# Optimization experiments

Measured on AMD Instinct MI355X. Metric: run time of the kernel, lower is better.

Reference implementation:

```python
import jax, jax.numpy as jnp
import numpy as np

B, NQ, NK = 2, 2048, 2048
QD, CD, H, DH = 1024, 768, 16, 64
INNER = H * DH


def setup_inputs() -> dict:
    key = jax.random.key(0)
    ks = jax.random.split(key, 8)
    x = jax.random.normal(ks[0], (B, NQ, QD), jnp.float32)
    context = jax.random.normal(ks[1], (B, NK, CD), jnp.float32)
    mask = jax.random.randint(ks[2], (B, 1, NQ, NK), 0, 2) > 0
    s = lambda d: 1.0 / np.sqrt(d)
    Wq = jax.random.normal(ks[3], (INNER, QD), jnp.float32) * s(QD)
    Wk = jax.random.normal(ks[4], (INNER, CD), jnp.float32) * s(CD)
    Wv = jax.random.normal(ks[5], (INNER, CD), jnp.float32) * s(CD)
    Wo = jax.random.normal(ks[6], (QD, INNER), jnp.float32) * s(INNER)
    bo = jax.random.normal(ks[7], (QD,), jnp.float32) * 0.01
    return {"x": x, "context": context, "mask": mask,
            "Wq": Wq, "Wk": Wk, "Wv": Wv, "Wo": Wo, "bo": bo}


def reference(x, context, mask, Wq, Wk, Wv, Wo, bo):
    scale = DH ** -0.5
    # QKV projections (Linear, no bias): [b, n, inner] -> [b, n, h, d]
    q = (x @ Wq.T).reshape(B, NQ, H, DH)
    k = (context @ Wk.T).reshape(B, NK, H, DH)
    v = (context @ Wv.T).reshape(B, NK, H, DH)
    # additive bias built from boolean mask (masked_fill with -finfo.max/2)
    max_neg = -jnp.finfo(q.dtype).max / 2
    bias = jnp.where(mask, jnp.zeros((), q.dtype), max_neg)  # [b,1,nq,nk]
    scores = jnp.einsum('bqhd,bkhd->bhqk', q, k) * scale + bias
    attn = jax.nn.softmax(scores, axis=-1)
    out = jnp.einsum('bhqk,bkhd->bqhd', attn, v).reshape(B, NQ, INNER)
    return out @ Wo.T + bo
```

## Files before the change

### kernel.cpp

```cpp
#include <hip/hip_runtime.h>
#include <float.h>
#include <stdint.h>

#define C_B     2
#define C_NQ    2048
#define C_NK    2048
#define C_QD    1024
#define C_CD    768
#define C_H     16
#define C_DH    64
#define C_INNER 1024

typedef __bf16 bf16;
typedef __attribute__((ext_vector_type(8))) __bf16 bf16x8;
typedef __attribute__((ext_vector_type(4))) __bf16 bf16x4;
typedef __attribute__((ext_vector_type(4))) float f32x4;
typedef __attribute__((ext_vector_type(16))) float f32x16;

#if __has_builtin(__builtin_amdgcn_exp2f)
#define EXP2(x) __builtin_amdgcn_exp2f(x)
#else
#define EXP2(x) __expf((x) * 0.69314718056f)
#endif

__device__ __forceinline__ void async_copy16(const bf16* g, bf16* l) {
  __builtin_amdgcn_global_load_lds(
      (const __attribute__((address_space(1))) void*)g,
      (__attribute__((address_space(3))) void*)l,
      16, 0, 0);
}

__global__ __launch_bounds__(256) void cvt_all(const float* __restrict__ s0, const float* __restrict__ s1,
                                               const float* __restrict__ s2, const float* __restrict__ s3,
                                               const float* __restrict__ s4, const float* __restrict__ s5,
                                               bf16* __restrict__ d0, bf16* __restrict__ d1,
                                               bf16* __restrict__ d2, bf16* __restrict__ d3,
                                               bf16* __restrict__ d4, bf16* __restrict__ d5) {
  const int stride = gridDim.x * blockDim.x;
  for (int idx = blockIdx.x * blockDim.x + threadIdx.x; idx < 2752512; idx += stride) {
    const float* src; bf16* dst; int loc;
    if      (idx < 1048576) { src = s0; dst = d0; loc = idx; }
    else if (idx < 1835008) { src = s1; dst = d1; loc = idx - 1048576; }
    else if (idx < 2097152) { src = s2; dst = d2; loc = idx - 1835008; }
    else if (idx < 2293760) { src = s3; dst = d3; loc = idx - 2097152; }
    else if (idx < 2490368) { src = s4; dst = d4; loc = idx - 2293760; }
    else                    { src = s5; dst = d5; loc = idx - 2490368; }
    float4 f = *(const float4*)&src[loc * 4];
    bf16x4 o = { (bf16)f.x, (bf16)f.y, (bf16)f.z, (bf16)f.w };
    *(bf16x4*)&dst[loc * 4] = o;
  }
}

__global__ __launch_bounds__(256) void pack_mask(const int* __restrict__ mask,
                                                 unsigned long long* __restrict__ mb,
                                                 int nwords) {
  const int wid  = (blockIdx.x * blockDim.x + threadIdx.x) >> 6;
  const int lane = threadIdx.x & 63;
  const int nw   = (gridDim.x * blockDim.x) >> 6;
  for (int w = wid; w < nwords; w += nw) {
    int v = mask[(size_t)w * 64 + lane];
    unsigned long long bb = __ballot(v != 0);
    if (lane == 0) mb[w] = bb;
  }
}

template <int OUTBF16, int HASBIAS>
__global__ __launch_bounds__(256) void gemm_bt(const bf16* __restrict__ A,
                                               const bf16* __restrict__ W,
                                               const float* __restrict__ bias,
                                               void* __restrict__ Cout,
                                               int M, int N, int K, float oscale,
                                               int ncut, bf16* __restrict__ Cout2) {
  __shared__ __align__(16) bf16 As[2][64 * 32];
  __shared__ __align__(16) bf16 Bs[2][128 * 32];

  const int t = threadIdx.x;
  const int w = t >> 6, lane = t & 63;
  const int l15 = lane & 15, lg = lane >> 4;
  const int wm = w >> 1, wn = w & 1;
  const int m0 = blockIdx.y * 64, n0 = blockIdx.x * 128;

  f32x4 acc[2][4] = {};

  const bf16* Ag  = A + (size_t)(m0 + w * 16 + (lane >> 2)) * K + (lane & 3) * 8;
  const bf16* Bg0 = W + (size_t)(n0 + w * 32 + (lane >> 2)) * K + (lane & 3) * 8;
  const bf16* Bg1 = W + (size_t)(n0 + w * 32 + 16 + (lane >> 2)) * K + (lane & 3) * 8;

  auto stage = [&](int nb, int k0) {
    async_copy16(Ag + k0, &As[nb][w * 512]);
    async_copy16(Bg0 + k0, &Bs[nb][w * 1024]);
    async_copy16(Bg1 + k0, &Bs[nb][w * 1024 + 512]);
  };

  stage(0, 0);
  int cur = 0;
  for (int k0 = 0; k0 < K; k0 += 32) {
    __syncthreads();
    if (k0 + 32 < K) stage(cur ^ 1, k0 + 32);

    bf16x8 af[2], bfv[4];
#pragma unroll
    for (int mi = 0; mi < 2; ++mi)
      af[mi] = *(const bf16x8*)&As[cur][(wm * 32 + mi * 16 + l15) * 32 + lg * 8];
#pragma unroll
    for (int ni = 0; ni < 4; ++ni)
      bfv[ni] = *(const bf16x8*)&Bs[cur][(wn * 64 + ni * 16 + l15) * 32 + lg * 8];
#pragma unroll
    for (int mi = 0; mi < 2; ++mi)
#pragma unroll
      for (int ni = 0; ni < 4; ++ni)
        acc[mi][ni] = __builtin_amdgcn_mfma_f32_16x16x32_bf16(af[mi], bfv[ni],
                                                              acc[mi][ni], 0, 0, 0);
    cur ^= 1;
  }

#pragma unroll
  for (int mi = 0; mi < 2; ++mi)
#pragma unroll
    for (int ni = 0; ni < 4; ++ni)
#pragma unroll
      for (int r = 0; r < 4; ++r) {
        const int row = m0 + wm * 32 + mi * 16 + lg * 4 + r;
        const int col = n0 + wn * 64 + ni * 16 + l15;
        float v = acc[mi][ni][r] * oscale;
        if (HASBIAS) v += bias[col];
        if (OUTBF16) {
          bf16* dst; int cc, str;
          if (col < ncut) { dst = (bf16*)Cout; cc = col; str = ncut; }
          else            { dst = Cout2; cc = col - ncut; str = N - ncut; }
          dst[(size_t)row * str + cc] = (bf16)v;
        } else {
          ((float*)Cout)[(size_t)row * N + col] = v;
        }
      }
}

__global__ __launch_bounds__(256) void vtrans(const bf16* __restrict__ V,
                                              bf16* __restrict__ Vt) {
  __shared__ __align__(16) bf16 T[64][80];
  const int kt = blockIdx.x, h = blockIdx.y, b = blockIdx.z;
  const int t = threadIdx.x;
  {
    const int kl = t >> 2, db = (t & 3) * 16;
    const bf16* src = &V[((size_t)(b * C_NK + kt * 64 + kl)) * C_INNER + h * 64 + db];
    *(bf16x8*)&T[kl][db]     = *(const bf16x8*)&src[0];
    *(bf16x8*)&T[kl][db + 8] = *(const bf16x8*)&src[8];
  }
  __syncthreads();
  {
    const int d = t >> 2, kb = (t & 3) * 16;
    const int P0[8] = {0, 1, 2, 3, 8, 9, 10, 11};
    const int P1[8] = {4, 5, 6, 7, 12, 13, 14, 15};
    bf16x8 o0, o1;
#pragma unroll
    for (int j = 0; j < 8; ++j) { o0[j] = T[kb + P0[j]][d]; o1[j] = T[kb + P1[j]][d]; }
    bf16* dst = &Vt[((size_t)((b * C_H + h) * C_DH + d)) * C_NK + kt * 64 + kb];
    *(bf16x8*)&dst[0] = o0;
    *(bf16x8*)&dst[8] = o1;
  }
}

#define KVB 32
__global__ __launch_bounds__(128, 4) void attn_fwd(const bf16* __restrict__ Q,
                                                   const bf16* __restrict__ K,
                                                   const bf16* __restrict__ Vt,
                                                   const unsigned long long* __restrict__ MB,
                                                   bf16* __restrict__ O0,
                                                   bf16* __restrict__ O1,
                                                   float2* __restrict__ LM) {
  __shared__ __align__(16) bf16 Ks[2][KVB * 64];
  __shared__ __align__(16) bf16 Vs[2][64 * KVB];

  const int qt = blockIdx.x, h = blockIdx.y;
  const int half = blockIdx.z >> 1, b = blockIdx.z & 1;
  const int t = threadIdx.x, wq = t >> 6, lane = t & 63;
  const int l31 = lane & 31, hi = lane >> 5;
  const int q = qt * 64 + wq * 32 + l31;

  bf16x8 qf[4];
  {
    const bf16* qp = Q + ((size_t)(b * C_NQ + q)) * C_INNER + h * C_DH;
#pragma unroll
    for (int db = 0; db < 4; ++db)
      qf[db] = *(const bf16x8*)&qp[db * 16 + hi * 8];
  }

  float m_run = -3.0e38f, l_run = 0.f;
  f32x16 acc_o[2] = {};

  auto stage = [&](int nb, int ktA) {
#pragma unroll
    for (int c = 0; c < 2; ++c) {
      const int chunk = wq * 128 + c * 64 + lane;
      const int krow = chunk >> 3, kpcb = chunk & 7;
      const int ksrc = (kpcb ^ (krow & 7)) * 8;
      const bf16* kg = K + ((size_t)(b * C_NK + ktA * KVB + krow)) * C_INNER + h * C_DH + ksrc;
      async_copy16(kg, &Ks[nb][chunk * 8]);
      const int vrow = chunk >> 2, vpcb = chunk & 3;
      const int vsrc = (vpcb ^ (vrow & 3)) * 8;
      const bf16* vg = Vt + ((size_t)((b * C_H + h) * C_DH + vrow)) * C_NK + ktA * KVB + vsrc;
      async_copy16(vg, &Vs[nb][chunk * 8]);
    }
  };

  const int kt0 = half * 32;
  stage(0, kt0);
  int cur = 0;

  for (int i = 0; i < 32; ++i) {
    const int ktA = kt0 + i;
    const unsigned mw = (unsigned)(
        MB[((size_t)(b * C_NQ + q)) * (C_NK / 64) + (ktA >> 1)] >>
        ((ktA & 1) * 32 + hi * 4));

    __syncthreads();
    if (i + 1 < 32) stage(cur ^ 1, ktA + 1);

    f32x16 s = {};
    __builtin_amdgcn_s_setprio(1);
#pragma unroll
    for (int db = 0; db < 4; ++db) {
      const int row = l31;
      const int cb = (db * 2 + hi) ^ (row & 7);
      bf16x8 kf = *(const bf16x8*)&Ks[cur][row * 64 + cb * 8];
      s = __builtin_amdgcn_mfma_f32_32x32x16_bf16(kf, qf[db], s, 0, 0, 0);
    }
    __builtin_amdgcn_s_setprio(0);

    float pm = -1.0e30f;
#pragma unroll
    for (int reg = 0; reg < 16; ++reg) pm = fmaxf(pm, s[reg]);
    pm = fmaxf(pm, __shfl_xor(pm, 32));

    if (!__all(pm <= m_run + 8.0f)) {
      const float mn = fmaxf(m_run, pm);
      const float f = EXP2(m_run - mn);
      m_run = mn;
      l_run *= f;
#pragma unroll
      for (int d2 = 0; d2 < 2; ++d2)
#pragma unroll
        for (int reg = 0; reg < 16; ++reg)
          acc_o[d2][reg] *= f;
    }

    bf16x8 pfr[2];
    float ps = 0.f;
#pragma unroll
    for (int kss = 0; kss < 2; ++kss) {
      bf16x8 pf;
#pragma unroll
      for (int j = 0; j < 8; ++j) {
        const int reg = kss * 8 + j;
        const int pos = (reg & 3) + 8 * (reg >> 2);
        float p = EXP2(s[reg] - m_run);
        p = ((mw >> pos) & 1u) ? p : 0.f;
        ps += p;
        pf[j] = (bf16)p;
      }
      pfr[kss] = pf;
    }
    l_run += ps;

    __builtin_amdgcn_s_setprio(1);
#pragma unroll
    for (int ks = 0; ks < 2; ++ks) {
#pragma unroll
      for (int d2 = 0; d2 < 2; ++d2) {
        const int row = d2 * 32 + l31;
        const int cb = (ks * 2 + hi) ^ (row & 3);
        bf16x8 vf = *(const bf16x8*)&Vs[cur][row * KVB + cb * 8];
        acc_o[d2] = __builtin_amdgcn_mfma_f32_32x32x16_bf16(vf, pfr[ks], acc_o[d2], 0, 0, 0);
      }
    }
    __builtin_amdgcn_s_setprio(0);
    cur ^= 1;
  }

  {
    const float l_tot = l_run + __shfl_xor(l_run, 32);
    const size_t row = (size_t)(b * C_H + h) * C_NQ + q;
    bf16* op = (half ? O1 : O0) + row * 64;
#pragma unroll
    for (int d2 = 0; d2 < 2; ++d2)
#pragma unroll
      for (int bb = 0; bb < 4; ++bb) {
        bf16x4 o;
#pragma unroll
        for (int rr = 0; rr < 4; ++rr)
          o[rr] = (bf16)(acc_o[d2][bb * 4 + rr]);
        *(bf16x4*)&op[d2 * 32 + bb * 8 + hi * 4] = o;
      }
    if (hi == 0) LM[(size_t)half * 65536 + row] = make_float2(m_run, l_tot);
  }
}

__global__ __launch_bounds__(256) void merge_halves(const bf16* __restrict__ O0,
                                                    const bf16* __restrict__ O1,
                                                    const float2* __restrict__ LM,
                                                    bf16* __restrict__ AO) {
  const int t = threadIdx.x;
  const int r = blockIdx.x * 32 + (t >> 3);
  const int dc = (t & 7) * 8;
  const float2 lm0 = LM[r], lm1 = LM[65536 + r];
  const float ms = fmaxf(lm0.x, lm1.x);
  const float w0 = EXP2(lm0.x - ms), w1 = EXP2(lm1.x - ms);
  const float denom = lm0.y * w0 + lm1.y * w1;
  const float s0 = w0 / denom, s1 = w1 / denom;
  bf16x8 a = *(const bf16x8*)&O0[(size_t)r * 64 + dc];
  bf16x8 c = *(const bf16x8*)&O1[(size_t)r * 64 + dc];
  bf16x8 o;
#pragma unroll
  for (int j = 0; j < 8; ++j)
    o[j] = (bf16)((float)a[j] * s0 + (float)c[j] * s1);
  const int q = r & 2047, bh = r >> 11, hh = bh & 15, bb = bh >> 4;
  *(bf16x8*)&AO[((size_t)(bb * C_NQ + q)) * C_INNER + hh * 64 + dc] = o;
}

extern "C" void kernel_launch(void* const* d_in, const int* in_sizes, int n_in,
                              void* d_out, int out_size, void* d_ws, size_t ws_size,
                              hipStream_t stream) {
  const float* x   = (const float*)d_in[0];
  const float* ctx = (const float*)d_in[1];
  const int*   msk = (const int*)d_in[2];
  const float* Wq  = (const float*)d_in[3];
  const float* Wk  = (const float*)d_in[4];
  const float* Wv  = (const float*)d_in[5];
  const float* Wo  = (const float*)d_in[6];
  const float* bo  = (const float*)d_in[7];
  float* out = (float*)d_out;

  bf16* ws  = (bf16*)d_ws;
  bf16* xb  = ws;
  bf16* cb  = xb  + 4194304;
  bf16* wqb = cb  + 3145728;
  bf16* wkb = wqb + 1048576;
  bf16* wvb = wkb + 786432;
  bf16* wob = wvb + 786432;
  bf16* Qb  = wob + 1048576;
  bf16* Kb  = Qb  + 4194304;
  bf16* Vb  = Kb  + 4194304;
  bf16* AOb = Vb  + 4194304;
  unsigned long long* mb = (unsigned long long*)(AOb + 4194304);
  float2* lm = (float2*)(mb + 131072);
  bf16* Vtb = xb;
  bf16* O0  = cb;
  bf16* O1  = Vb;

  dim3 blk(256);
  cvt_all<<<2048, blk, 0, stream>>>(x, ctx, Wq, Wk, Wv, Wo, xb, cb, wqb, wkb, wvb, wob);

  pack_mask<<<512, blk, 0, stream>>>(msk, mb, C_B * C_NQ * (C_NK / 64));

  const int MQ = C_B * C_NQ;
  const float qscale = 0.125f * 1.44269504f;
  gemm_bt<1, 0><<<dim3(C_INNER / 128, MQ / 64), blk, 0, stream>>>(
      xb, wqb, nullptr, Qb, MQ, C_INNER, C_QD, qscale, C_INNER, nullptr);
  gemm_bt<1, 0><<<dim3(2 * C_INNER / 128, MQ / 64), blk, 0, stream>>>(
      cb, wkb, nullptr, Kb, MQ, 2 * C_INNER, C_CD, 1.0f, C_INNER, Vb);

  vtrans<<<dim3(C_NK / 64, C_H, C_B), blk, 0, stream>>>(Vb, Vtb);

  attn_fwd<<<dim3(C_NQ / 64, C_H, 2 * C_B), dim3(128), 0, stream>>>(
      Qb, Kb, Vtb, mb, O0, O1, lm);

  merge_halves<<<2048, blk, 0, stream>>>(O0, O1, lm, AOb);

  gemm_bt<0, 1><<<dim3(C_QD / 128, MQ / 64), blk, 0, stream>>>(
      AOb, wob, bo, out, MQ, C_QD, C_INNER, 1.0f, C_QD, nullptr);
}
```

Before: 178.7 us.

## Enlarge GEMM and attention tiles to 128 rows with swizzled LDS

The projection GEMM tile grows from 64x128 to 128x128. Each warp now computes a 64x64 sub-tile with 16 MFMA accumulators, and shared memory uses an XOR swizzle to avoid bank conflicts. The attention kernel moves to 256 threads covering 128 queries and processes 64-key blocks per iteration, 16 iterations per half instead of 32. Larger tiles are meant to cut global loads per FLOP, barriers and loop overhead, at the cost of more registers, fewer blocks and possibly lower occupancy.

```diff
diff --git a/kernel.cpp b/kernel.cpp
--- a/kernel.cpp
+++ b/kernel.cpp
@@ -71,25 +71,26 @@
                                                void* __restrict__ Cout,
                                                int M, int N, int K, float oscale,
                                                int ncut, bf16* __restrict__ Cout2) {
-  __shared__ __align__(16) bf16 As[2][64 * 32];
+  __shared__ __align__(16) bf16 As[2][128 * 32];
   __shared__ __align__(16) bf16 Bs[2][128 * 32];
 
   const int t = threadIdx.x;
   const int w = t >> 6, lane = t & 63;
   const int l15 = lane & 15, lg = lane >> 4;
   const int wm = w >> 1, wn = w & 1;
-  const int m0 = blockIdx.y * 64, n0 = blockIdx.x * 128;
-
-  f32x4 acc[2][4] = {};
-
-  const bf16* Ag  = A + (size_t)(m0 + w * 16 + (lane >> 2)) * K + (lane & 3) * 8;
-  const bf16* Bg0 = W + (size_t)(n0 + w * 32 + (lane >> 2)) * K + (lane & 3) * 8;
-  const bf16* Bg1 = W + (size_t)(n0 + w * 32 + 16 + (lane >> 2)) * K + (lane & 3) * 8;
+  const int m0 = blockIdx.y * 128, n0 = blockIdx.x * 128;
+
+  f32x4 acc[4][4] = {};
 
   auto stage = [&](int nb, int k0) {
-    async_copy16(Ag + k0, &As[nb][w * 512]);
-    async_copy16(Bg0 + k0, &Bs[nb][w * 1024]);
-    async_copy16(Bg1 + k0, &Bs[nb][w * 1024 + 512]);
+#pragma unroll
+    for (int i = 0; i < 2; ++i) {
+      const int chunk = w * 128 + i * 64 + lane;
+      const int row = chunk >> 2;
+      const int srcb = ((chunk & 3) ^ (row & 3)) * 8;
+      async_copy16(A + (size_t)(m0 + row) * K + k0 + srcb, &As[nb][chunk * 8]);
+      async_copy16(W + (size_t)(n0 + row) * K + k0 + srcb, &Bs[nb][chunk * 8]);
+    }
   };
 
   stage(0, 0);
@@ -98,15 +99,19 @@
     __syncthreads();
     if (k0 + 32 < K) stage(cur ^ 1, k0 + 32);
 
-    bf16x8 af[2], bfv[4];
-#pragma unroll
-    for (int mi = 0; mi < 2; ++mi)
-      af[mi] = *(const bf16x8*)&As[cur][(wm * 32 + mi * 16 + l15) * 32 + lg * 8];
-#pragma unroll
-    for (int ni = 0; ni < 4; ++ni)
-      bfv[ni] = *(const bf16x8*)&Bs[cur][(wn * 64 + ni * 16 + l15) * 32 + lg * 8];
-#pragma unroll
-    for (int mi = 0; mi < 2; ++mi)
+    bf16x8 af[4], bfv[4];
+#pragma unroll
+    for (int mi = 0; mi < 4; ++mi) {
+      const int row = wm * 64 + mi * 16 + l15;
+      af[mi] = *(const bf16x8*)&As[cur][row * 32 + ((lg ^ (row & 3)) * 8)];
+    }
+#pragma unroll
+    for (int ni = 0; ni < 4; ++ni) {
+      const int row = wn * 64 + ni * 16 + l15;
+      bfv[ni] = *(const bf16x8*)&Bs[cur][row * 32 + ((lg ^ (row & 3)) * 8)];
+    }
+#pragma unroll
+    for (int mi = 0; mi < 4; ++mi)
 #pragma unroll
       for (int ni = 0; ni < 4; ++ni)
         acc[mi][ni] = __builtin_amdgcn_mfma_f32_16x16x32_bf16(af[mi], bfv[ni],
@@ -115,12 +120,12 @@
   }
 
 #pragma unroll
-  for (int mi = 0; mi < 2; ++mi)
+  for (int mi = 0; mi < 4; ++mi)
 #pragma unroll
     for (int ni = 0; ni < 4; ++ni)
 #pragma unroll
       for (int r = 0; r < 4; ++r) {
-        const int row = m0 + wm * 32 + mi * 16 + lg * 4 + r;
+        const int row = m0 + wm * 64 + mi * 16 + lg * 4 + r;
         const int col = n0 + wn * 64 + ni * 16 + l15;
         float v = acc[mi][ni][r] * oscale;
         if (HASBIAS) v += bias[col];
@@ -160,22 +165,21 @@
   }
 }
 
-#define KVB 32
-__global__ __launch_bounds__(128, 4) void attn_fwd(const bf16* __restrict__ Q,
+__global__ __launch_bounds__(256, 4) void attn_fwd(const bf16* __restrict__ Q,
                                                    const bf16* __restrict__ K,
                                                    const bf16* __restrict__ Vt,
                                                    const unsigned long long* __restrict__ MB,
                                                    bf16* __restrict__ O0,
                                                    bf16* __restrict__ O1,
                                                    float2* __restrict__ LM) {
-  __shared__ __align__(16) bf16 Ks[2][KVB * 64];
-  __shared__ __align__(16) bf16 Vs[2][64 * KVB];
+  __shared__ __align__(16) bf16 Ks[2][64 * 64];
+  __shared__ __align__(16) bf16 Vs[2][64 * 64];
 
   const int qt = blockIdx.x, h = blockIdx.y;
   const int half = blockIdx.z >> 1, b = blockIdx.z & 1;
   const int t = threadIdx.x, wq = t >> 6, lane = t & 63;
   const int l31 = lane & 31, hi = lane >> 5;
-  const int q = qt * 64 + wq * 32 + l31;
+  const int q = qt * 128 + wq * 32 + l31;
 
   bf16x8 qf[4];
   {
@@ -190,46 +194,48 @@
 
   auto stage = [&](int nb, int ktA) {
 #pragma unroll
-    for (int c = 0; c < 2; ++c) {
-      const int chunk = wq * 128 + c * 64 + lane;
-      const int krow = chunk >> 3, kpcb = chunk & 7;
-      const int ksrc = (kpcb ^ (krow & 7)) * 8;
-      const bf16* kg = K + ((size_t)(b * C_NK + ktA * KVB + krow)) * C_INNER + h * C_DH + ksrc;
+    for (int i = 0; i < 2; ++i) {
+      const int chunk = wq * 128 + i * 64 + lane;
+      const int row = chunk >> 3, pcb = chunk & 7;
+      const int srcb = (pcb ^ (row & 7)) * 8;
+      const bf16* kg = K + ((size_t)(b * C_NK + ktA * 64 + row)) * C_INNER + h * C_DH + srcb;
       async_copy16(kg, &Ks[nb][chunk * 8]);
-      const int vrow = chunk >> 2, vpcb = chunk & 3;
-      const int vsrc = (vpcb ^ (vrow & 3)) * 8;
-      const bf16* vg = Vt + ((size_t)((b * C_H + h) * C_DH + vrow)) * C_NK + ktA * KVB + vsrc;
+      const bf16* vg = Vt + ((size_t)((b * C_H + h) * C_DH + row)) * C_NK + ktA * 64 + srcb;
       async_copy16(vg, &Vs[nb][chunk * 8]);
     }
   };
 
-  const int kt0 = half * 32;
+  const int kt0 = half * 16;
   stage(0, kt0);
   int cur = 0;
 
-  for (int i = 0; i < 32; ++i) {
+  for (int i = 0; i < 16; ++i) {
     const int ktA = kt0 + i;
-    const unsigned mw = (unsigned)(
-        MB[((size_t)(b * C_NQ + q)) * (C_NK / 64) + (ktA >> 1)] >>
-        ((ktA & 1) * 32 + hi * 4));
+    const unsigned long long wd =
+        MB[((size_t)(b * C_NQ + q)) * (C_NK / 64) + ktA] >> (hi * 4);
+    const unsigned mlo = (unsigned)wd, mhi = (unsigned)(wd >> 32);
 
     __syncthreads();
-    if (i + 1 < 32) stage(cur ^ 1, ktA + 1);
-
-    f32x16 s = {};
+    if (i + 1 < 16) stage(cur ^ 1, ktA + 1);
+
+    f32x16 s[2] = {};
     __builtin_amdgcn_s_setprio(1);
 #pragma unroll
-    for (int db = 0; db < 4; ++db) {
-      const int row = l31;
-      const int cb = (db * 2 + hi) ^ (row & 7);
-      bf16x8 kf = *(const bf16x8*)&Ks[cur][row * 64 + cb * 8];
-      s = __builtin_amdgcn_mfma_f32_32x32x16_bf16(kf, qf[db], s, 0, 0, 0);
-    }
+    for (int kb = 0; kb < 2; ++kb)
+#pragma unroll
+      for (int db = 0; db < 4; ++db) {
+        const int row = kb * 32 + l31;
+        const int cb = (db * 2 + hi) ^ (row & 7);
+        bf16x8 kf = *(const bf16x8*)&Ks[cur][row * 64 + cb * 8];
+        s[kb] = __builtin_amdgcn_mfma_f32_32x32x16_bf16(kf, qf[db], s[kb], 0, 0, 0);
+      }
     __builtin_amdgcn_s_setprio(0);
 
     float pm = -1.0e30f;
 #pragma unroll
-    for (int reg = 0; reg < 16; ++reg) pm = fmaxf(pm, s[reg]);
+    for (int kb = 0; kb < 2; ++kb)
+#pragma unroll
+      for (int reg = 0; reg < 16; ++reg) pm = fmaxf(pm, s[kb][reg]);
     pm = fmaxf(pm, __shfl_xor(pm, 32));
 
     if (!__all(pm <= m_run + 8.0f)) {
@@ -244,32 +250,36 @@
           acc_o[d2][reg] *= f;
     }
 
-    bf16x8 pfr[2];
+    bf16x8 pfr[4];
     float ps = 0.f;
 #pragma unroll
-    for (int kss = 0; kss < 2; ++kss) {
-      bf16x8 pf;
-#pragma unroll
-      for (int j = 0; j < 8; ++j) {
-        const int reg = kss * 8 + j;
-        const int pos = (reg & 3) + 8 * (reg >> 2);
-        float p = EXP2(s[reg] - m_run);
-        p = ((mw >> pos) & 1u) ? p : 0.f;
-        ps += p;
-        pf[j] = (bf16)p;
-      }
-      pfr[kss] = pf;
+    for (int kb = 0; kb < 2; ++kb) {
+      const unsigned mw = kb ? mhi : mlo;
+#pragma unroll
+      for (int kss = 0; kss < 2; ++kss) {
+        bf16x8 pf;
+#pragma unroll
+        for (int j = 0; j < 8; ++j) {
+          const int reg = kss * 8 + j;
+          const int pos = (reg & 3) + 8 * (reg >> 2);
+          float p = EXP2(s[kb][reg] - m_run);
+          p = ((mw >> pos) & 1u) ? p : 0.f;
+          ps += p;
+          pf[j] = (bf16)p;
+        }
+        pfr[kb * 2 + kss] = pf;
+      }
     }
     l_run += ps;
 
     __builtin_amdgcn_s_setprio(1);
 #pragma unroll
-    for (int ks = 0; ks < 2; ++ks) {
+    for (int ks = 0; ks < 4; ++ks) {
 #pragma unroll
       for (int d2 = 0; d2 < 2; ++d2) {
         const int row = d2 * 32 + l31;
-        const int cb = (ks * 2 + hi) ^ (row & 3);
-        bf16x8 vf = *(const bf16x8*)&Vs[cur][row * KVB + cb * 8];
+        const int cb = (ks * 2 + hi) ^ (row & 7);
+        bf16x8 vf = *(const bf16x8*)&Vs[cur][row * 64 + cb * 8];
         acc_o[d2] = __builtin_amdgcn_mfma_f32_32x32x16_bf16(vf, pfr[ks], acc_o[d2], 0, 0, 0);
       }
     }
@@ -354,18 +364,18 @@
 
   const int MQ = C_B * C_NQ;
   const float qscale = 0.125f * 1.44269504f;
-  gemm_bt<1, 0><<<dim3(C_INNER / 128, MQ / 64), blk, 0, stream>>>(
+  gemm_bt<1, 0><<<dim3(C_INNER / 128, MQ / 128), blk, 0, stream>>>(
       xb, wqb, nullptr, Qb, MQ, C_INNER, C_QD, qscale, C_INNER, nullptr);
-  gemm_bt<1, 0><<<dim3(2 * C_INNER / 128, MQ / 64), blk, 0, stream>>>(
+  gemm_bt<1, 0><<<dim3(2 * C_INNER / 128, MQ / 128), blk, 0, stream>>>(
       cb, wkb, nullptr, Kb, MQ, 2 * C_INNER, C_CD, 1.0f, C_INNER, Vb);
 
   vtrans<<<dim3(C_NK / 64, C_H, C_B), blk, 0, stream>>>(Vb, Vtb);
 
-  attn_fwd<<<dim3(C_NQ / 64, C_H, 2 * C_B), dim3(128), 0, stream>>>(
+  attn_fwd<<<dim3(C_NQ / 128, C_H, 2 * C_B), blk, 0, stream>>>(
       Qb, Kb, Vtb, mb, O0, O1, lm);
 
   merge_halves<<<2048, blk, 0, stream>>>(O0, O1, lm, AOb);
 
-  gemm_bt<0, 1><<<dim3(C_QD / 128, MQ / 64), blk, 0, stream>>>(
+  gemm_bt<0, 1><<<dim3(C_QD / 128, MQ / 128), blk, 0, stream>>>(
       AOb, wob, bo, out, MQ, C_QD, C_INNER, 1.0f, C_QD, nullptr);
 }
```

Result: faster. 173.4 us (-2.9%).
